# Kernel tuning notes

Measured on AMD Instinct MI355X. Metric: run time of the kernel, lower is better.

Reference implementation:

```python
import jax, jax.numpy as jnp
import numpy as np

EPS = 1e-06

def setup_inputs() -> dict:
    key = jax.random.key(0)
    k1, k2, k3, k4, k5 = jax.random.split(key, 5)
    B, S, H = 4, 4096, 4096
    x1 = jax.random.normal(k1, (B, S, H), dtype=jnp.float32)
    x2 = jax.random.normal(k2, (B, S, H), dtype=jnp.float32)
    gamma = jax.random.uniform(k3, (H,), dtype=jnp.float32)
    smooth_scale1 = jax.random.uniform(k4, (H,), dtype=jnp.float32)
    smooth_scale2 = jax.random.uniform(k5, (H,), dtype=jnp.float32)
    return {"x1": x1, "x2": x2, "gamma": gamma,
            "smooth_scale1": smooth_scale1, "smooth_scale2": smooth_scale2}

def reference(x1, x2, gamma, smooth_scale1, smooth_scale2):
    # residual add
    x = x1 + x2
    # per-row RMS over last dim
    x_rms = jnp.sqrt(jnp.mean(x * x, axis=-1, keepdims=True) + EPS)
    output = (x / x_rms) * gamma
    # dynamic int8 quantization with a single global abs-max scale
    # (the original computes max_val twice; it is the same value)
    max_val = jnp.max(jnp.abs(output))
    scale1 = max_val / 127.0
    y1 = jnp.clip(jnp.round(output / scale1), -128, 127).astype(jnp.int8)
    scale2 = max_val / 127.0
    y2 = jnp.clip(jnp.round(output / scale2), -128, 127).astype(jnp.int8)
    return (y1, y2, x, scale1, scale2)
```

## Files before the change

### kernel.cpp

```cpp
#include <hip/hip_runtime.h>

#define HDIM 4096
#define NROWS 16384
#define TPB 256
#define EPS_RMS 1e-6f

__device__ __forceinline__ float wave_reduce_sum(float v) {
    #pragma unroll
    for (int off = 32; off > 0; off >>= 1)
        v += __shfl_down(v, off, 64);
    return v;
}
__device__ __forceinline__ float wave_reduce_max(float v) {
    #pragma unroll
    for (int off = 32; off > 0; off >>= 1)
        v = fmaxf(v, __shfl_down(v, off, 64));
    return v;
}

__global__ __launch_bounds__(TPB) void pass1_kernel(
    const float4* __restrict__ x1, const float4* __restrict__ x2,
    const float4* __restrict__ gamma, float4* __restrict__ xout,
    float* __restrict__ inv_rms, unsigned int* __restrict__ gmax) {
    const int row = blockIdx.x;
    const int t   = threadIdx.x;
    const size_t rowbase = (size_t)row * (HDIM / 4);

    float ss = 0.f;
    float gm = 0.f;
    #pragma unroll
    for (int k = 0; k < 4; ++k) {
        const int idx = t + k * TPB;
        float4 a = x1[rowbase + idx];
        float4 b = x2[rowbase + idx];
        float4 v;
        v.x = a.x + b.x; v.y = a.y + b.y; v.z = a.z + b.z; v.w = a.w + b.w;
        xout[rowbase + idx] = v;
        ss += v.x * v.x + v.y * v.y + v.z * v.z + v.w * v.w;
        float4 g = gamma[idx];
        gm = fmaxf(gm, fabsf(v.x * g.x));
        gm = fmaxf(gm, fabsf(v.y * g.y));
        gm = fmaxf(gm, fabsf(v.z * g.z));
        gm = fmaxf(gm, fabsf(v.w * g.w));
    }

    __shared__ float red_s[4];
    __shared__ float red_m[4];
    const int wave = t >> 6, lane = t & 63;
    float wsum = wave_reduce_sum(ss);
    float wmax = wave_reduce_max(gm);
    if (lane == 0) { red_s[wave] = wsum; red_m[wave] = wmax; }
    __syncthreads();
    if (t == 0) {
        float tot = (red_s[0] + red_s[1]) + (red_s[2] + red_s[3]);
        float inv = rsqrtf(tot * (1.0f / HDIM) + EPS_RMS);
        inv_rms[row] = inv;
        float m = fmaxf(fmaxf(red_m[0], red_m[1]), fmaxf(red_m[2], red_m[3])) * inv;
        atomicMax(gmax, __float_as_uint(m));
    }
}

__global__ __launch_bounds__(TPB) void pass2_kernel(
    const float4* __restrict__ x, const float4* __restrict__ gamma,
    const float* __restrict__ inv_rms, const unsigned int* __restrict__ gmax,
    float4* __restrict__ y1, float4* __restrict__ y2,
    float* __restrict__ scales) {
    const int row = blockIdx.x;
    const int t   = threadIdx.x;
    const float inv  = inv_rms[row];
    const float maxv = __uint_as_float(*gmax);
    const float qs   = 127.0f / maxv;
    const float c    = inv * qs;
    if (row == 0 && t == 0) {
        float scale = maxv * (1.0f / 127.0f);
        scales[0] = scale;
        scales[1] = scale;
    }
    const size_t rowbase = (size_t)row * (HDIM / 4);
    #pragma unroll
    for (int k = 0; k < 4; ++k) {
        const int idx = t + k * TPB;
        float4 v = x[rowbase + idx];
        float4 g = gamma[idx];
        float4 q;
        q.x = fminf(fmaxf(rintf(v.x * g.x * c), -128.f), 127.f);
        q.y = fminf(fmaxf(rintf(v.y * g.y * c), -128.f), 127.f);
        q.z = fminf(fmaxf(rintf(v.z * g.z * c), -128.f), 127.f);
        q.w = fminf(fmaxf(rintf(v.w * g.w * c), -128.f), 127.f);
        y1[rowbase + idx] = q;
        y2[rowbase + idx] = q;
    }
}

extern "C" void kernel_launch(void* const* d_in, const int* in_sizes, int n_in,
                              void* d_out, int out_size, void* d_ws, size_t ws_size,
                              hipStream_t stream) {
    const float* x1    = (const float*)d_in[0];
    const float* x2    = (const float*)d_in[1];
    const float* gamma = (const float*)d_in[2];

    const size_t N = (size_t)NROWS * HDIM;
    float* out    = (float*)d_out;
    float* y1     = out;
    float* y2     = out + N;
    float* xo     = out + 2 * N;
    float* scales = out + 3 * N;

    unsigned int* gmax = (unsigned int*)d_ws;
    float* inv_rms     = (float*)((char*)d_ws + 16);

    hipMemsetAsync(d_ws, 0, 16, stream);

    pass1_kernel<<<NROWS, TPB, 0, stream>>>(
        (const float4*)x1, (const float4*)x2, (const float4*)gamma,
        (float4*)xo, inv_rms, gmax);

    pass2_kernel<<<NROWS, TPB, 0, stream>>>(
        (const float4*)xo, (const float4*)gamma, inv_rms, gmax,
        (float4*)y1, (float4*)y2, scales);
}
```

Before: 1.181 ms.

## Fuse both passes into one cooperative persistent kernel with grid sync

Replaces the two-kernel pipeline with a single cooperative kernel of 1024 blocks, each handling 16 rows. A grid-wide sync separates the reduction phase from the quantize phase. Per-row inverse RMS now lives in shared memory and gamma is held in registers. Each block contributes one atomicMax instead of one per row. The second phase walks rows in reverse so the most recently written x rows may still be in cache, and it uses nontemporal loads and stores for streaming data. The cost is a grid barrier and a dependence on cooperative launch occupancy (4 blocks per CU).

```diff
diff --git a/kernel.cpp b/kernel.cpp
--- a/kernel.cpp
+++ b/kernel.cpp
@@ -1,9 +1,16 @@
 #include <hip/hip_runtime.h>
+#include <hip/hip_cooperative_groups.h>
 
 #define HDIM 4096
 #define NROWS 16384
 #define TPB 256
+#define GRID 1024
+#define RPB (NROWS / GRID)
 #define EPS_RMS 1e-6f
+
+namespace cg = cooperative_groups;
+
+typedef float f32x4 __attribute__((ext_vector_type(4)));
 
 __device__ __forceinline__ float wave_reduce_sum(float v) {
     #pragma unroll
@@ -18,104 +25,109 @@
     return v;
 }
 
-__global__ __launch_bounds__(TPB) void pass1_kernel(
-    const float4* __restrict__ x1, const float4* __restrict__ x2,
-    const float4* __restrict__ gamma, float4* __restrict__ xout,
-    float* __restrict__ inv_rms, unsigned int* __restrict__ gmax) {
-    const int row = blockIdx.x;
-    const int t   = threadIdx.x;
-    const size_t rowbase = (size_t)row * (HDIM / 4);
+__global__ __launch_bounds__(TPB, 4) void fused_kernel(
+    const f32x4* __restrict__ x1, const f32x4* __restrict__ x2,
+    const f32x4* __restrict__ gamma, f32x4* __restrict__ xout,
+    f32x4* __restrict__ y1, f32x4* __restrict__ y2,
+    float* __restrict__ scales, unsigned int* __restrict__ gmax)
+{
+    const int t    = threadIdx.x;
+    const int wave = t >> 6, lane = t & 63;
+    __shared__ float red_s[2][4], red_m[2][4];
+    __shared__ float inv_s[RPB];
 
-    float ss = 0.f;
-    float gm = 0.f;
+    f32x4 g[4];
     #pragma unroll
-    for (int k = 0; k < 4; ++k) {
-        const int idx = t + k * TPB;
-        float4 a = x1[rowbase + idx];
-        float4 b = x2[rowbase + idx];
-        float4 v;
-        v.x = a.x + b.x; v.y = a.y + b.y; v.z = a.z + b.z; v.w = a.w + b.w;
-        xout[rowbase + idx] = v;
-        ss += v.x * v.x + v.y * v.y + v.z * v.z + v.w * v.w;
-        float4 g = gamma[idx];
-        gm = fmaxf(gm, fabsf(v.x * g.x));
-        gm = fmaxf(gm, fabsf(v.y * g.y));
-        gm = fmaxf(gm, fabsf(v.z * g.z));
-        gm = fmaxf(gm, fabsf(v.w * g.w));
+    for (int k = 0; k < 4; ++k) g[k] = gamma[t + k * TPB];
+
+    float blkmax = 0.f;
+
+    #pragma unroll 1
+    for (int r = 0; r < RPB; ++r) {
+        const int row = blockIdx.x * RPB + r;
+        const size_t rowbase = (size_t)row * (HDIM / 4);
+        float ss = 0.f, gm = 0.f;
+        #pragma unroll
+        for (int k = 0; k < 4; ++k) {
+            const int idx = t + k * TPB;
+            f32x4 a = __builtin_nontemporal_load(&x1[rowbase + idx]);
+            f32x4 b = __builtin_nontemporal_load(&x2[rowbase + idx]);
+            f32x4 v = a + b;
+            xout[rowbase + idx] = v;
+            ss += v.x * v.x + v.y * v.y + v.z * v.z + v.w * v.w;
+            f32x4 ag = v * g[k];
+            gm = fmaxf(gm, fmaxf(fmaxf(fabsf(ag.x), fabsf(ag.y)),
+                                 fmaxf(fabsf(ag.z), fabsf(ag.w))));
+        }
+        float wsum = wave_reduce_sum(ss);
+        float wmax = wave_reduce_max(gm);
+        if (lane == 0) { red_s[r & 1][wave] = wsum; red_m[r & 1][wave] = wmax; }
+        __syncthreads();
+        if (t == 0) {
+            float tot = (red_s[r & 1][0] + red_s[r & 1][1])
+                      + (red_s[r & 1][2] + red_s[r & 1][3]);
+            float inv = rsqrtf(tot * (1.0f / HDIM) + EPS_RMS);
+            inv_s[r] = inv;
+            float m = fmaxf(fmaxf(red_m[r & 1][0], red_m[r & 1][1]),
+                            fmaxf(red_m[r & 1][2], red_m[r & 1][3])) * inv;
+            blkmax = fmaxf(blkmax, m);
+        }
+    }
+    if (t == 0) atomicMax(gmax, __float_as_uint(blkmax));
+
+    cg::this_grid().sync();
+
+    const unsigned int mu =
+        __hip_atomic_load(gmax, __ATOMIC_RELAXED, __HIP_MEMORY_SCOPE_AGENT);
+    const float maxv = __uint_as_float(mu);
+    const float qs   = 127.0f / maxv;
+    if (blockIdx.x == 0 && t == 0) {
+        float s = maxv * (1.0f / 127.0f);
+        scales[0] = s;
+        scales[1] = s;
     }
 
-    __shared__ float red_s[4];
-    __shared__ float red_m[4];
-    const int wave = t >> 6, lane = t & 63;
-    float wsum = wave_reduce_sum(ss);
-    float wmax = wave_reduce_max(gm);
-    if (lane == 0) { red_s[wave] = wsum; red_m[wave] = wmax; }
-    __syncthreads();
-    if (t == 0) {
-        float tot = (red_s[0] + red_s[1]) + (red_s[2] + red_s[3]);
-        float inv = rsqrtf(tot * (1.0f / HDIM) + EPS_RMS);
-        inv_rms[row] = inv;
-        float m = fmaxf(fmaxf(red_m[0], red_m[1]), fmaxf(red_m[2], red_m[3])) * inv;
-        atomicMax(gmax, __float_as_uint(m));
-    }
-}
-
-__global__ __launch_bounds__(TPB) void pass2_kernel(
-    const float4* __restrict__ x, const float4* __restrict__ gamma,
-    const float* __restrict__ inv_rms, const unsigned int* __restrict__ gmax,
-    float4* __restrict__ y1, float4* __restrict__ y2,
-    float* __restrict__ scales) {
-    const int row = blockIdx.x;
-    const int t   = threadIdx.x;
-    const float inv  = inv_rms[row];
-    const float maxv = __uint_as_float(*gmax);
-    const float qs   = 127.0f / maxv;
-    const float c    = inv * qs;
-    if (row == 0 && t == 0) {
-        float scale = maxv * (1.0f / 127.0f);
-        scales[0] = scale;
-        scales[1] = scale;
-    }
-    const size_t rowbase = (size_t)row * (HDIM / 4);
-    #pragma unroll
-    for (int k = 0; k < 4; ++k) {
-        const int idx = t + k * TPB;
-        float4 v = x[rowbase + idx];
-        float4 g = gamma[idx];
-        float4 q;
-        q.x = fminf(fmaxf(rintf(v.x * g.x * c), -128.f), 127.f);
-        q.y = fminf(fmaxf(rintf(v.y * g.y * c), -128.f), 127.f);
-        q.z = fminf(fmaxf(rintf(v.z * g.z * c), -128.f), 127.f);
-        q.w = fminf(fmaxf(rintf(v.w * g.w * c), -128.f), 127.f);
-        y1[rowbase + idx] = q;
-        y2[rowbase + idx] = q;
+    #pragma unroll 1
+    for (int r = RPB - 1; r >= 0; --r) {
+        const int row = blockIdx.x * RPB + r;
+        const size_t rowbase = (size_t)row * (HDIM / 4);
+        const float c = inv_s[r] * qs;
+        #pragma unroll
+        for (int k = 0; k < 4; ++k) {
+            const int idx = t + k * TPB;
+            f32x4 v = __builtin_nontemporal_load(&xout[rowbase + idx]);
+            f32x4 q;
+            q.x = fminf(fmaxf(rintf(v.x * g[k].x * c), -128.f), 127.f);
+            q.y = fminf(fmaxf(rintf(v.y * g[k].y * c), -128.f), 127.f);
+            q.z = fminf(fmaxf(rintf(v.z * g[k].z * c), -128.f), 127.f);
+            q.w = fminf(fmaxf(rintf(v.w * g[k].w * c), -128.f), 127.f);
+            __builtin_nontemporal_store(q, &y1[rowbase + idx]);
+            __builtin_nontemporal_store(q, &y2[rowbase + idx]);
+        }
     }
 }
 
 extern "C" void kernel_launch(void* const* d_in, const int* in_sizes, int n_in,
                               void* d_out, int out_size, void* d_ws, size_t ws_size,
                               hipStream_t stream) {
-    const float* x1    = (const float*)d_in[0];
-    const float* x2    = (const float*)d_in[1];
-    const float* gamma = (const float*)d_in[2];
+    (void)in_sizes; (void)n_in; (void)out_size; (void)ws_size;
+    const f32x4* x1    = (const f32x4*)d_in[0];
+    const f32x4* x2    = (const f32x4*)d_in[1];
+    const f32x4* gamma = (const f32x4*)d_in[2];
 
     const size_t N = (size_t)NROWS * HDIM;
-    float* out    = (float*)d_out;
-    float* y1     = out;
-    float* y2     = out + N;
-    float* xo     = out + 2 * N;
+    float* out   = (float*)d_out;
+    f32x4* y1    = (f32x4*)out;
+    f32x4* y2    = (f32x4*)(out + N);
+    f32x4* xo    = (f32x4*)(out + 2 * N);
     float* scales = out + 3 * N;
 
     unsigned int* gmax = (unsigned int*)d_ws;
-    float* inv_rms     = (float*)((char*)d_ws + 16);
 
     hipMemsetAsync(d_ws, 0, 16, stream);
 
-    pass1_kernel<<<NROWS, TPB, 0, stream>>>(
-        (const float4*)x1, (const float4*)x2, (const float4*)gamma,
-        (float4*)xo, inv_rms, gmax);
-
-    pass2_kernel<<<NROWS, TPB, 0, stream>>>(
-        (const float4*)xo, (const float4*)gamma, inv_rms, gmax,
-        (float4*)y1, (float4*)y2, scales);
+    void* args[8] = { (void*)&x1, (void*)&x2, (void*)&gamma, (void*)&xo,
+                      (void*)&y1, (void*)&y2, (void*)&scales, (void*)&gmax };
+    hipLaunchCooperativeKernel((const void*)fused_kernel,
+                               dim3(GRID), dim3(TPB), args, 0u, stream);
 }
```

Result: slower. 1.254 ms (+6.2%).
